# Performance work log

Hardware: AMD Instinct MI355X
Metric: run time of the kernel (lower is better)

The kernel has to match this reference:

```python
import jax, jax.numpy as jnp
import numpy as np

EPS = 1e-7
MAX_NORM = 1.0 - 1e-3  # projection radius of the unit Poincare ball (c=1)
ALPHA = 0.2            # LeakyReLU negative slope
NEG_INF = -9e15


def _proj(x, max_norm=MAX_NORM):
    # Project points back inside the Poincare ball along the last dim.
    norm = jnp.clip(jnp.linalg.norm(x, axis=-1, keepdims=True), EPS)
    return jnp.where(norm > max_norm, x / norm * max_norm, x)


def _logmap0(x):
    # Log map at the origin of the Poincare ball, c = 1.
    norm = jnp.clip(jnp.linalg.norm(x, axis=-1, keepdims=True), EPS, 1.0 - EPS)
    return jnp.arctanh(norm) * x / norm


def _expmap0(v):
    # Exp map at the origin of the Poincare ball, c = 1.
    norm = jnp.clip(jnp.linalg.norm(v, axis=-1, keepdims=True), EPS)
    return jnp.tanh(norm) * v / norm


def setup_inputs() -> dict:
    key = jax.random.key(0)
    k1, k2, k3 = jax.random.split(key, 3)
    N, D = 12288, 128
    # points strictly inside the ball: ||x|| ~ 0.01*sqrt(128) ~ 0.11 < 1
    x = jax.random.normal(k1, (N, D), dtype=jnp.float32) * 0.01
    adj = jax.random.randint(k2, (N, N), 0, 2, dtype=jnp.int32)
    # attention vector a, as in init: N(0, 0.2) then proj(a, 0.9) row-wise
    a = jax.random.normal(k3, (2 * D, 1), dtype=jnp.float32) * 0.2
    a = _proj(a, 0.9)
    return {"x": x, "adj": adj, "a": a}


def reference(x, adj, a):
    D = a.shape[0] // 2
    x_tan = _logmap0(x)                       # [N, D]
    wh1 = x_tan @ a[:D]                       # [N, 1]
    wh2 = x_tan @ a[D:]                       # [N, 1]
    e = jax.nn.leaky_relu(wh1 + wh2.T, ALPHA)  # [N, N] additive scores
    scores = jnp.where(adj > 0, e, NEG_INF)
    attention = jax.nn.softmax(scores, axis=1)  # dropout omitted (eval mode)
    x_tan_prime = attention @ x_tan            # [N, D]
    return _proj(_expmap0(x_tan_prime))
```

## Files before the change

### kernel.cpp

```cpp
#include <hip/hip_runtime.h>
#include <math.h>

#define NN 12288
#define DD 128
#define EPSF 1e-7f
#define MAXNORM (1.0f - 1e-3f)

#define TI 32
#define TJ 64
#define LDP 72

typedef __attribute__((ext_vector_type(8))) short short8_t;
typedef __attribute__((ext_vector_type(4))) float float4_t;
typedef unsigned short ushort_t;

__device__ __forceinline__ unsigned short f2bf(float f) {
    unsigned int u = __builtin_bit_cast(unsigned int, f);
    unsigned int r = u + 0x7FFFu + ((u >> 16) & 1u);
    return (unsigned short)(r >> 16);
}

__global__ __launch_bounds__(128) void prep_kernel(
    const float* __restrict__ x, const float* __restrict__ a,
    ushort_t* __restrict__ xtb,
    float* __restrict__ wh1, float* __restrict__ wh2,
    float* __restrict__ e1, float* __restrict__ e1b,
    float* __restrict__ ey, float* __restrict__ ez)
{
    const int r = blockIdx.x;
    const int t = threadIdx.x;
    const float xv = x[r * DD + t];
    const float a1 = a[t];
    const float a2 = a[DD + t];
    float s0 = xv * xv, s1 = xv * a1, s2 = xv * a2;
    #pragma unroll
    for (int o = 32; o > 0; o >>= 1) {
        s0 += __shfl_xor(s0, o);
        s1 += __shfl_xor(s1, o);
        s2 += __shfl_xor(s2, o);
    }
    __shared__ float red[6];
    const int w = t >> 6;
    if ((t & 63) == 0) { red[w * 3 + 0] = s0; red[w * 3 + 1] = s1; red[w * 3 + 2] = s2; }
    __syncthreads();
    const float sumsq = red[0] + red[3];
    const float d1    = red[1] + red[4];
    const float d2    = red[2] + red[5];
    const float nraw  = sqrtf(sumsq);
    const float nrm   = fminf(fmaxf(nraw, EPSF), 1.0f - EPSF);
    const float scale = atanhf(nrm) / nrm;
    xtb[(size_t)r * DD + t] = f2bf(xv * scale);
    if (t == 0) {
        const float w1 = scale * d1;
        const float w2 = scale * d2;
        wh1[r] = w1; wh2[r] = w2;
        e1[r]  = expf(w1);
        e1b[r] = expf(0.2f * w1);
        ey[r]  = expf(w2);
        ez[r]  = expf(0.2f * w2);
    }
}

__global__ __launch_bounds__(256) void transpose_kernel(
    const ushort_t* __restrict__ xtb, ushort_t* __restrict__ xtT)
{
    __shared__ ushort_t tile[64][65];
    const int j0 = blockIdx.x * 64;
    const int d0 = blockIdx.y * 64;
    const int t = threadIdx.x;
    const int c = t & 63, r4 = t >> 6;
    #pragma unroll
    for (int k = 0; k < 16; ++k) {
        const int jj = r4 + 4 * k;
        tile[jj][c] = xtb[(size_t)(j0 + jj) * DD + d0 + c];
    }
    __syncthreads();
    #pragma unroll
    for (int k = 0; k < 16; ++k) {
        const int dd = r4 + 4 * k;
        xtT[(size_t)(d0 + dd) * NN + j0 + c] = tile[c][dd];
    }
}

__global__ __launch_bounds__(256) void attn_kernel(
    const int* __restrict__ adj,
    const ushort_t* __restrict__ xtT,
    const float* __restrict__ wh1, const float* __restrict__ e1,
    const float* __restrict__ e1b,
    const float* __restrict__ wh2, const float* __restrict__ ey,
    const float* __restrict__ ez,
    float* __restrict__ pout, float* __restrict__ plsum, int jlen)
{
    __shared__ __align__(16) ushort_t xtT_lds[DD * LDP];
    __shared__ __align__(16) ushort_t p_lds[TI * LDP];
    __shared__ float s_wh1[TI], s_e1[TI], s_e1b[TI];

    const int t = threadIdx.x;
    const int i0 = blockIdx.x * TI;
    const int s  = blockIdx.y;
    const int jbase = s * jlen;
    const int lane = t & 63;
    const int w = t >> 6;
    const int l15 = lane & 15;
    const int quad = lane >> 4;
    const int ihalf = w & 1;
    const int dgrp = w >> 1;

    if (t < TI) {
        s_wh1[t] = wh1[i0 + t];
        s_e1[t]  = e1[i0 + t];
        s_e1b[t] = e1b[i0 + t];
    }

    float4_t acc[4];
    #pragma unroll
    for (int dt = 0; dt < 4; ++dt) acc[dt] = (float4_t)0.0f;
    float pls[8];
    #pragma unroll
    for (int k = 0; k < 8; ++k) pls[k] = 0.0f;

    for (int j0 = jbase; j0 < jbase + jlen; j0 += TJ) {
        __syncthreads();

        #pragma unroll
        for (int c = 0; c < 4; ++c) {
            const int idx = c * 256 + t;
            const int row = idx >> 3;
            const int ch  = idx & 7;
            const uint4 v = *(const uint4*)(xtT + (size_t)row * NN + j0 + ch * 8);
            *(uint4*)(&xtT_lds[row * LDP + ch * 8]) = v;
        }

        {
            const float w2j = wh2[j0 + lane];
            const float eyj = ey[j0 + lane];
            const float ezj = ez[j0 + lane];
            const int* ap = adj + (size_t)(i0 + w * 8) * NN + j0 + lane;
            #pragma unroll
            for (int k = 0; k < 8; ++k) {
                const int il = w * 8 + k;
                const int av = ap[(size_t)k * NN];
                float p = 0.0f;
                if (av > 0) {
                    const bool cpos = (s_wh1[il] + w2j) > 0.0f;
                    p = cpos ? s_e1[il] * eyj : s_e1b[il] * ezj;
                }
                pls[k] += p;
                p_lds[il * LDP + lane] = f2bf(p);
            }
        }
        __syncthreads();

        #pragma unroll
        for (int kc = 0; kc < 2; ++kc) {
            const short8_t af = *(const short8_t*)(
                &p_lds[(ihalf * 16 + l15) * LDP + kc * 32 + quad * 8]);
            #pragma unroll
            for (int dt = 0; dt < 4; ++dt) {
                const short8_t bf = *(const short8_t*)(
                    &xtT_lds[((dgrp * 4 + dt) * 16 + l15) * LDP + kc * 32 + quad * 8]);
                acc[dt] = __builtin_amdgcn_mfma_f32_16x16x32_bf16(af, bf, acc[dt], 0, 0, 0);
            }
        }
    }

    #pragma unroll
    for (int k = 0; k < 8; ++k) {
        float v = pls[k];
        #pragma unroll
        for (int o = 1; o < 64; o <<= 1) v += __shfl_xor(v, o);
        if (lane == 0) plsum[(size_t)s * NN + i0 + w * 8 + k] = v;
    }

    #pragma unroll
    for (int dt = 0; dt < 4; ++dt) {
        const int d = (dgrp * 4 + dt) * 16 + l15;
        #pragma unroll
        for (int reg = 0; reg < 4; ++reg) {
            const int i = i0 + ihalf * 16 + quad * 4 + reg;
            pout[((size_t)s * NN + i) * DD + d] = acc[dt][reg];
        }
    }
}

__global__ __launch_bounds__(128) void reduce_kernel(
    const float* __restrict__ pout, const float* __restrict__ plsum,
    float* __restrict__ out, int S)
{
    const int i = blockIdx.x;
    const int t = threadIdx.x;
    float v = 0.0f;
    for (int s = 0; s < S; ++s) v += pout[((size_t)s * NN + i) * DD + t];
    float ls = 0.0f;
    for (int s = 0; s < S; ++s) ls += plsum[(size_t)s * NN + i];
    v /= ls;
    float ss = v * v;
    #pragma unroll
    for (int o = 1; o < 64; o <<= 1) ss += __shfl_xor(ss, o);
    __shared__ float r2[2];
    if ((t & 63) == 0) r2[t >> 6] = ss;
    __syncthreads();
    const float total = r2[0] + r2[1];
    const float nraw = sqrtf(total);
    const float nv   = fmaxf(nraw, EPSF);
    const float th   = tanhf(nv);
    const float ysc  = th / nv;
    const float nyr  = ysc * nraw;
    const float ny   = fmaxf(nyr, EPSF);
    const float psc  = (ny > MAXNORM) ? (MAXNORM / ny) : 1.0f;
    const float os   = ysc * psc;
    out[(size_t)i * DD + t] = v * os;
}

extern "C" void kernel_launch(void* const* d_in, const int* in_sizes, int n_in,
                              void* d_out, int out_size, void* d_ws, size_t ws_size,
                              hipStream_t stream) {
    const float* x   = (const float*)d_in[0];
    const int*   adj = (const int*)d_in[1];
    const float* a   = (const float*)d_in[2];
    float* out = (float*)d_out;

    char* ws = (char*)d_ws;
    ushort_t* xtb = (ushort_t*)ws;  ws += (size_t)NN * DD * sizeof(ushort_t);
    ushort_t* xtT = (ushort_t*)ws;  ws += (size_t)DD * NN * sizeof(ushort_t);
    float* wh1 = (float*)ws;        ws += NN * sizeof(float);
    float* wh2 = (float*)ws;        ws += NN * sizeof(float);
    float* e1  = (float*)ws;        ws += NN * sizeof(float);
    float* e1b = (float*)ws;        ws += NN * sizeof(float);
    float* eyv = (float*)ws;        ws += NN * sizeof(float);
    float* ezv = (float*)ws;        ws += NN * sizeof(float);

    const size_t fixed = (size_t)(ws - (char*)d_ws);
    const size_t perS  = (size_t)NN * DD * sizeof(float) + NN * sizeof(float);
    int S = 1;
    const int cand[5] = {8, 6, 4, 3, 2};
    for (int c = 0; c < 5; ++c) {
        if (fixed + (size_t)cand[c] * perS <= ws_size) { S = cand[c]; break; }
    }
    float* plsum = (float*)ws;      ws += (size_t)S * NN * sizeof(float);
    float* pout  = (float*)ws;

    const int jlen = NN / S;

    prep_kernel<<<NN, 128, 0, stream>>>(x, a, xtb, wh1, wh2, e1, e1b, eyv, ezv);
    transpose_kernel<<<dim3(NN / 64, DD / 64), 256, 0, stream>>>(xtb, xtT);
    attn_kernel<<<dim3(NN / TI, S), 256, 0, stream>>>(
        adj, xtT, wh1, e1, e1b, wh2, eyv, ezv, pout, plsum, jlen);
    reduce_kernel<<<NN, 128, 0, stream>>>(pout, plsum, out, S);
}
```

Before: 1.024 ms.

## Restructure attention kernel to register-direct MFMA operands without LDS staging

Rewrites the attention kernel so that each wave owns 16 rows and all 128 output columns. Each lane loads its adjacency values and wh2 with 128-bit loads and computes probabilities directly in registers as the MFMA A-operand. The xtT B-operands are read straight from global memory, which removes the LDS staging and both block barriers per tile. The precomputed exponent factorisation is replaced by a per-element __expf, the split count S can now go up to 16, and launch bounds request 3 blocks per CU. In exchange, xtT reads are no longer shared through LDS across the four waves, so each wave reads global or cache separately, and register pressure rises with 8 accumulators plus 16 B fragments.

```diff
diff --git a/kernel.cpp b/kernel.cpp
--- a/kernel.cpp
+++ b/kernel.cpp
@@ -6,10 +6,6 @@
 #define EPSF 1e-7f
 #define MAXNORM (1.0f - 1e-3f)
 
-#define TI 32
-#define TJ 64
-#define LDP 72
-
 typedef __attribute__((ext_vector_type(8))) short short8_t;
 typedef __attribute__((ext_vector_type(4))) float float4_t;
 typedef unsigned short ushort_t;
@@ -23,9 +19,7 @@
 __global__ __launch_bounds__(128) void prep_kernel(
     const float* __restrict__ x, const float* __restrict__ a,
     ushort_t* __restrict__ xtb,
-    float* __restrict__ wh1, float* __restrict__ wh2,
-    float* __restrict__ e1, float* __restrict__ e1b,
-    float* __restrict__ ey, float* __restrict__ ez)
+    float* __restrict__ wh1, float* __restrict__ wh2)
 {
     const int r = blockIdx.x;
     const int t = threadIdx.x;
@@ -51,13 +45,8 @@
     const float scale = atanhf(nrm) / nrm;
     xtb[(size_t)r * DD + t] = f2bf(xv * scale);
     if (t == 0) {
-        const float w1 = scale * d1;
-        const float w2 = scale * d2;
-        wh1[r] = w1; wh2[r] = w2;
-        e1[r]  = expf(w1);
-        e1b[r] = expf(0.2f * w1);
-        ey[r]  = expf(w2);
-        ez[r]  = expf(0.2f * w2);
+        wh1[r] = scale * d1;
+        wh2[r] = scale * d2;
     }
 }
 
@@ -82,103 +71,93 @@
     }
 }
 
-__global__ __launch_bounds__(256) void attn_kernel(
+__device__ __forceinline__ void p8(
+    const int4& Aa, const int4& Ab, const float4& Wa, const float4& Wb,
+    float wh1i, float& lsum, unsigned short pr[8])
+{
+    const int   av[8] = {Aa.x, Aa.y, Aa.z, Aa.w, Ab.x, Ab.y, Ab.z, Ab.w};
+    const float wv[8] = {Wa.x, Wa.y, Wa.z, Wa.w, Wb.x, Wb.y, Wb.z, Wb.w};
+    #pragma unroll
+    for (int j = 0; j < 8; ++j) {
+        const float u  = wh1i + wv[j];
+        const float lr = fmaxf(u, 0.2f * u);
+        float p = 0.0f;
+        if (av[j] > 0) p = __expf(lr);
+        lsum += p;
+        pr[j] = f2bf(p);
+    }
+}
+
+__global__ __launch_bounds__(256, 3) void attn_kernel(
     const int* __restrict__ adj,
     const ushort_t* __restrict__ xtT,
-    const float* __restrict__ wh1, const float* __restrict__ e1,
-    const float* __restrict__ e1b,
-    const float* __restrict__ wh2, const float* __restrict__ ey,
-    const float* __restrict__ ez,
+    const float* __restrict__ wh1, const float* __restrict__ wh2,
     float* __restrict__ pout, float* __restrict__ plsum, int jlen)
 {
-    __shared__ __align__(16) ushort_t xtT_lds[DD * LDP];
-    __shared__ __align__(16) ushort_t p_lds[TI * LDP];
-    __shared__ float s_wh1[TI], s_e1[TI], s_e1b[TI];
-
-    const int t = threadIdx.x;
-    const int i0 = blockIdx.x * TI;
-    const int s  = blockIdx.y;
-    const int jbase = s * jlen;
+    const int t = threadIdx.x;
+    const int w = t >> 6;
     const int lane = t & 63;
-    const int w = t >> 6;
     const int l15 = lane & 15;
     const int quad = lane >> 4;
-    const int ihalf = w & 1;
-    const int dgrp = w >> 1;
-
-    if (t < TI) {
-        s_wh1[t] = wh1[i0 + t];
-        s_e1[t]  = e1[i0 + t];
-        s_e1b[t] = e1b[i0 + t];
-    }
-
-    float4_t acc[4];
-    #pragma unroll
-    for (int dt = 0; dt < 4; ++dt) acc[dt] = (float4_t)0.0f;
-    float pls[8];
-    #pragma unroll
-    for (int k = 0; k < 8; ++k) pls[k] = 0.0f;
-
-    for (int j0 = jbase; j0 < jbase + jlen; j0 += TJ) {
-        __syncthreads();
-
-        #pragma unroll
-        for (int c = 0; c < 4; ++c) {
-            const int idx = c * 256 + t;
-            const int row = idx >> 3;
-            const int ch  = idx & 7;
-            const uint4 v = *(const uint4*)(xtT + (size_t)row * NN + j0 + ch * 8);
-            *(uint4*)(&xtT_lds[row * LDP + ch * 8]) = v;
+    const int i0 = blockIdx.x * 64;
+    const int s = blockIdx.y;
+    const int jbase = s * jlen;
+    const int iw = i0 + w * 16 + l15;
+
+    const float wh1i = wh1[iw];
+
+    float4_t acc[8];
+    #pragma unroll
+    for (int dt = 0; dt < 8; ++dt) acc[dt] = (float4_t)0.0f;
+    float lsum = 0.0f;
+
+    const int* adj_row = adj + (size_t)iw * NN;
+
+    for (int j0 = jbase; j0 < jbase + jlen; j0 += 64) {
+        const int4* ap = (const int4*)(adj_row + j0);
+        const int4 A0 = ap[quad * 2 + 0];
+        const int4 A1 = ap[quad * 2 + 1];
+        const int4 A2 = ap[quad * 2 + 8];
+        const int4 A3 = ap[quad * 2 + 9];
+        const float4* wp = (const float4*)(wh2 + j0);
+        const float4 W0 = wp[quad * 2 + 0];
+        const float4 W1 = wp[quad * 2 + 1];
+        const float4 W2 = wp[quad * 2 + 8];
+        const float4 W3 = wp[quad * 2 + 9];
+
+        short8_t bf0[8], bf1[8];
+        #pragma unroll
+        for (int dt = 0; dt < 8; ++dt) {
+            const ushort_t* bp = xtT + (size_t)(dt * 16 + l15) * NN + j0 + quad * 8;
+            bf0[dt] = *(const short8_t*)bp;
+            bf1[dt] = *(const short8_t*)(bp + 32);
         }
 
-        {
-            const float w2j = wh2[j0 + lane];
-            const float eyj = ey[j0 + lane];
-            const float ezj = ez[j0 + lane];
-            const int* ap = adj + (size_t)(i0 + w * 8) * NN + j0 + lane;
-            #pragma unroll
-            for (int k = 0; k < 8; ++k) {
-                const int il = w * 8 + k;
-                const int av = ap[(size_t)k * NN];
-                float p = 0.0f;
-                if (av > 0) {
-                    const bool cpos = (s_wh1[il] + w2j) > 0.0f;
-                    p = cpos ? s_e1[il] * eyj : s_e1b[il] * ezj;
-                }
-                pls[k] += p;
-                p_lds[il * LDP + lane] = f2bf(p);
-            }
-        }
-        __syncthreads();
-
-        #pragma unroll
-        for (int kc = 0; kc < 2; ++kc) {
-            const short8_t af = *(const short8_t*)(
-                &p_lds[(ihalf * 16 + l15) * LDP + kc * 32 + quad * 8]);
-            #pragma unroll
-            for (int dt = 0; dt < 4; ++dt) {
-                const short8_t bf = *(const short8_t*)(
-                    &xtT_lds[((dgrp * 4 + dt) * 16 + l15) * LDP + kc * 32 + quad * 8]);
-                acc[dt] = __builtin_amdgcn_mfma_f32_16x16x32_bf16(af, bf, acc[dt], 0, 0, 0);
-            }
-        }
-    }
-
-    #pragma unroll
-    for (int k = 0; k < 8; ++k) {
-        float v = pls[k];
-        #pragma unroll
-        for (int o = 1; o < 64; o <<= 1) v += __shfl_xor(v, o);
-        if (lane == 0) plsum[(size_t)s * NN + i0 + w * 8 + k] = v;
-    }
-
-    #pragma unroll
-    for (int dt = 0; dt < 4; ++dt) {
-        const int d = (dgrp * 4 + dt) * 16 + l15;
+        unsigned short pr0[8], pr1[8];
+        p8(A0, A1, W0, W1, wh1i, lsum, pr0);
+        p8(A2, A3, W2, W3, wh1i, lsum, pr1);
+        short8_t af0, af1;
+        #pragma unroll
+        for (int j = 0; j < 8; ++j) { af0[j] = (short)pr0[j]; af1[j] = (short)pr1[j]; }
+
+        #pragma unroll
+        for (int dt = 0; dt < 8; ++dt)
+            acc[dt] = __builtin_amdgcn_mfma_f32_16x16x32_bf16(af0, bf0[dt], acc[dt], 0, 0, 0);
+        #pragma unroll
+        for (int dt = 0; dt < 8; ++dt)
+            acc[dt] = __builtin_amdgcn_mfma_f32_16x16x32_bf16(af1, bf1[dt], acc[dt], 0, 0, 0);
+    }
+
+    lsum += __shfl_xor(lsum, 16);
+    lsum += __shfl_xor(lsum, 32);
+    if (quad == 0) plsum[(size_t)s * NN + iw] = lsum;
+
+    #pragma unroll
+    for (int dt = 0; dt < 8; ++dt) {
         #pragma unroll
         for (int reg = 0; reg < 4; ++reg) {
-            const int i = i0 + ihalf * 16 + quad * 4 + reg;
-            pout[((size_t)s * NN + i) * DD + d] = acc[dt][reg];
+            const int i = i0 + w * 16 + quad * 4 + reg;
+            pout[((size_t)s * NN + i) * DD + dt * 16 + l15] = acc[dt][reg];
         }
     }
 }
@@ -225,16 +204,12 @@
     ushort_t* xtT = (ushort_t*)ws;  ws += (size_t)DD * NN * sizeof(ushort_t);
     float* wh1 = (float*)ws;        ws += NN * sizeof(float);
     float* wh2 = (float*)ws;        ws += NN * sizeof(float);
-    float* e1  = (float*)ws;        ws += NN * sizeof(float);
-    float* e1b = (float*)ws;        ws += NN * sizeof(float);
-    float* eyv = (float*)ws;        ws += NN * sizeof(float);
-    float* ezv = (float*)ws;        ws += NN * sizeof(float);
 
     const size_t fixed = (size_t)(ws - (char*)d_ws);
     const size_t perS  = (size_t)NN * DD * sizeof(float) + NN * sizeof(float);
     int S = 1;
-    const int cand[5] = {8, 6, 4, 3, 2};
-    for (int c = 0; c < 5; ++c) {
+    const int cand[7] = {16, 12, 8, 6, 4, 3, 2};
+    for (int c = 0; c < 7; ++c) {
         if (fixed + (size_t)cand[c] * perS <= ws_size) { S = cand[c]; break; }
     }
     float* plsum = (float*)ws;      ws += (size_t)S * NN * sizeof(float);
@@ -242,9 +217,9 @@
 
     const int jlen = NN / S;
 
-    prep_kernel<<<NN, 128, 0, stream>>>(x, a, xtb, wh1, wh2, e1, e1b, eyv, ezv);
+    prep_kernel<<<NN, 128, 0, stream>>>(x, a, xtb, wh1, wh2);
     transpose_kernel<<<dim3(NN / 64, DD / 64), 256, 0, stream>>>(xtb, xtT);
-    attn_kernel<<<dim3(NN / TI, S), 256, 0, stream>>>(
-        adj, xtT, wh1, e1, e1b, wh2, eyv, ezv, pout, plsum, jlen);
+    attn_kernel<<<dim3(NN / 64, S), 256, 0, stream>>>(
+        adj, xtT, wh1, wh2, pout, plsum, jlen);
     reduce_kernel<<<NN, 128, 0, stream>>>(pout, plsum, out, S);
 }
```

After: 1.047 ms. +2.2%, slower.
